# Performance work log

Measured on AMD Instinct MI355X. Metric: run time of the kernel, lower is better.

## Reference

```python
import jax, jax.numpy as jnp
import numpy as np

B, S, D, K = 4, 4096, 1024, 4
EPS = 1e-6


def rmsnorm(x, w):
    # x: [..., D]; matches torch RMSNorm: x * rsqrt(mean(x^2) + eps) * w
    n = jax.lax.rsqrt(jnp.mean(x * x, axis=-1, keepdims=True) + EPS)
    return x * n * w


def setup_inputs() -> dict:
    key = jax.random.key(0)
    ks = jax.random.split(key, 6)
    return {
        "x": jax.random.normal(ks[0], (B, S, D), jnp.float32),
        "norm_w": jnp.ones((D,), jnp.float32),
        "in_w": jax.random.normal(ks[1], (D, 2 * D), jnp.float32) / np.sqrt(D).astype(np.float32),
        "conv_w": jax.random.normal(ks[2], (D, 1, K), jnp.float32) / np.sqrt(K).astype(np.float32),
        "conv_b": jnp.zeros((D,), jnp.float32),
        "decay": jax.random.normal(ks[3], (D,), jnp.float32),
        "gate_w": jnp.ones((D,), jnp.float32),
        "out_w": jax.random.normal(ks[4], (D, D), jnp.float32) / np.sqrt(D).astype(np.float32),
        "res_scale": jnp.ones((1,), jnp.float32),
    }


def reference(x, norm_w, in_w, conv_w, conv_b, decay, gate_w, out_w, res_scale):
    residual = x
    h = rmsnorm(x, norm_w)
    xz = jnp.einsum("bsd,de->bse", h, in_w)          # [B,S,2D]
    xb, z = jnp.split(xz, 2, axis=-1)                  # each [B,S,D]

    # depthwise causal conv1d (left pad K-1, truncate to S)
    xc = jax.lax.conv_general_dilated(
        xb.transpose(0, 2, 1), conv_w,
        window_strides=(1,), padding=[(K - 1, 0)],
        feature_group_count=D,
        dimension_numbers=("NCH", "OIH", "NCH"))
    xc = (xc + conv_b[None, :, None]).transpose(0, 2, 1)  # [B,S,D]
    xc = jax.nn.silu(xc)

    # RNN cell: diagonal linear recurrence h_t = a * h_{t-1} + x_t
    a = jax.nn.sigmoid(decay)                          # [D]

    def step(hprev, xt):
        hnew = a * hprev + xt
        return hnew, hnew

    h0 = jnp.zeros((B, D), xc.dtype)
    _, hs = jax.lax.scan(step, h0, xc.transpose(1, 0, 2))  # [S,B,D]
    hs = hs.transpose(1, 0, 2)                             # [B,S,D]

    y = rmsnorm(hs, gate_w) * jax.nn.silu(z)
    y = jnp.einsum("bsd,de->bse", y, out_w)
    return residual * res_scale + y
```

## Files before the change

kernel.cpp:

```cpp
#include <hip/hip_runtime.h>
#include <cstddef>

#define BATCH 4
#define SEQ   4096
#define DIM   1024
#define KCONV 4
#define EPSV  1e-6f
#define MROWS (BATCH * SEQ)
#define CHUNK 32
#define NCHUNK (SEQ / CHUNK)

using short8v = __attribute__((ext_vector_type(8))) short;
using f32x4   = __attribute__((ext_vector_type(4))) float;

__device__ __forceinline__ unsigned short f2bf_rne(float f) {
  unsigned int u = __float_as_uint(f);
  u += 0x7FFFu + ((u >> 16) & 1u);
  return (unsigned short)(u >> 16);
}
__device__ __forceinline__ float bf2f(unsigned short h) {
  return __uint_as_float((unsigned int)h << 16);
}

__device__ __forceinline__ float wave_reduce_sum(float v) {
#pragma unroll
  for (int off = 32; off > 0; off >>= 1)
    v += __shfl_xor(v, off, 64);
  return v;
}

__global__ __launch_bounds__(256) void splitx_kernel(
    const float* __restrict__ x, const float* __restrict__ norm_w,
    unsigned short* __restrict__ Xhi, unsigned short* __restrict__ Xlo) {
  const int row = blockIdx.x * 4 + (threadIdx.x >> 6);
  const int lane = threadIdx.x & 63;
  float4 v[4];
  float ss = 0.f;
#pragma unroll
  for (int i = 0; i < 4; ++i) {
    v[i] = *reinterpret_cast<const float4*>(
        &x[(size_t)row * DIM + lane * 4 + i * 256]);
    ss += v[i].x * v[i].x + v[i].y * v[i].y + v[i].z * v[i].z + v[i].w * v[i].w;
  }
  const float rstd = rsqrtf(wave_reduce_sum(ss) * (1.0f / DIM) + EPSV);
#pragma unroll
  for (int i = 0; i < 4; ++i) {
    const int d4 = lane * 4 + i * 256;
    const float4 w = *reinterpret_cast<const float4*>(&norm_w[d4]);
    const float hv[4] = {v[i].x * rstd * w.x, v[i].y * rstd * w.y,
                         v[i].z * rstd * w.z, v[i].w * rstd * w.w};
    ushort4 hh, ll;
    hh.x = f2bf_rne(hv[0]); ll.x = f2bf_rne(hv[0] - bf2f(hh.x));
    hh.y = f2bf_rne(hv[1]); ll.y = f2bf_rne(hv[1] - bf2f(hh.y));
    hh.z = f2bf_rne(hv[2]); ll.z = f2bf_rne(hv[2] - bf2f(hh.z));
    hh.w = f2bf_rne(hv[3]); ll.w = f2bf_rne(hv[3] - bf2f(hh.w));
    *reinterpret_cast<ushort4*>(&Xhi[(size_t)row * DIM + d4]) = hh;
    *reinterpret_cast<ushort4*>(&Xlo[(size_t)row * DIM + d4]) = ll;
  }
}

__global__ __launch_bounds__(256) void splitw_kernel(
    const float* __restrict__ W, unsigned short* __restrict__ Whi,
    unsigned short* __restrict__ Wlo, int K, int N) {
  __shared__ float t[32][33];
  const int n0 = blockIdx.x * 32, k0 = blockIdx.y * 32;
  const int c = threadIdx.x & 31, r = threadIdx.x >> 5;
#pragma unroll
  for (int i = 0; i < 4; ++i)
    t[r + i * 8][c] = W[(size_t)(k0 + r + i * 8) * N + n0 + c];
  __syncthreads();
#pragma unroll
  for (int i = 0; i < 4; ++i) {
    const int n = n0 + r + i * 8, k = k0 + c;
    const float v = t[c][r + i * 8];
    const unsigned short h = f2bf_rne(v);
    Whi[(size_t)n * K + k] = h;
    Wlo[(size_t)n * K + k] = f2bf_rne(v - bf2f(h));
  }
}

template <int NT, bool RESID, bool OBF16>
__global__ __launch_bounds__(256) void gemm_kernel(
    const unsigned short* __restrict__ Ahi, const unsigned short* __restrict__ Alo,
    const unsigned short* __restrict__ Bhi, const unsigned short* __restrict__ Blo,
    float* __restrict__ Cf, unsigned short* __restrict__ Ch, int N, int lda,
    const float* __restrict__ resid, const float* __restrict__ res_scale) {
  __shared__ __align__(16) unsigned short lds[NT * 4096];

  const int tid = threadIdx.x;
  const int lane = tid & 63;
  const int wr = tid >> 7;
  const int wc = (tid >> 6) & 1;

  const int nwg = gridDim.x * gridDim.y;
  int id = blockIdx.y * gridDim.x + blockIdx.x;
  id = (id & 7) * (nwg >> 3) + (id >> 3);
  const int bx = id % gridDim.x;
  const int by = id / gridDim.x;
  const int bm = by * 128;
  const int bn = bx * 128;

  const unsigned short* pg[2 * NT];
  unsigned int lofs[2 * NT];
#pragma unroll
  for (int i = 0; i < 2 * NT; ++i) {
    const int o = tid * 16 + i * 4096;
    const int t = o >> 13;
    const int ot = o & 8191;
    const int b = ot ^ (((ot >> 7) & 7) << 4);
    const int r = b >> 6;
    const int ck = (b & 63) >> 1;
    const unsigned short* base;
    bool aside;
    if constexpr (NT == 4) {
      base = (t == 0) ? Ahi : (t == 1) ? Alo : (t == 2) ? Bhi : Blo;
      aside = (t < 2);
    } else {
      base = (t == 0) ? Ahi : Bhi;
      aside = (t < 1);
    }
    const int stride = aside ? lda : 1024;
    const int rowg = (aside ? bm : bn) + r;
    pg[i] = base + (size_t)rowg * stride + ck;
    lofs[i] = (unsigned int)(o >> 1);
  }

  unsigned int aoff[4], boff[4];
#pragma unroll
  for (int i = 0; i < 4; ++i) {
    int ba = (wr * 64 + i * 16 + (lane & 15)) * 64 + (lane >> 4) * 16;
    ba ^= ((ba >> 7) & 7) << 4;
    aoff[i] = (unsigned int)(ba >> 1);
    int bb = (wc * 64 + i * 16 + (lane & 15)) * 64 + (lane >> 4) * 16;
    bb ^= ((bb >> 7) & 7) << 4;
    boff[i] = (unsigned int)(bb >> 1) + (NT / 2) * 4096;
  }

  f32x4 acc[4][4];
#pragma unroll
  for (int mi = 0; mi < 4; ++mi)
#pragma unroll
    for (int ni = 0; ni < 4; ++ni) {
      acc[mi][ni][0] = 0.f; acc[mi][ni][1] = 0.f;
      acc[mi][ni][2] = 0.f; acc[mi][ni][3] = 0.f;
    }

  for (int k0 = 0; k0 < 1024; k0 += 32) {
#pragma unroll
    for (int i = 0; i < 2 * NT; ++i)
      __builtin_amdgcn_global_load_lds(
          (const __attribute__((address_space(1))) void*)(pg[i] + k0),
          (__attribute__((address_space(3))) void*)(&lds[lofs[i]]), 16, 0, 0);
    __syncthreads();

    short8v bh[4], bl[4];
#pragma unroll
    for (int ni = 0; ni < 4; ++ni) {
      bh[ni] = *reinterpret_cast<const short8v*>(&lds[boff[ni]]);
      if constexpr (NT == 4)
        bl[ni] = *reinterpret_cast<const short8v*>(&lds[boff[ni] + 4096]);
    }
#pragma unroll
    for (int mi = 0; mi < 4; ++mi) {
      const short8v ah = *reinterpret_cast<const short8v*>(&lds[aoff[mi]]);
#pragma unroll
      for (int ni = 0; ni < 4; ++ni)
        acc[mi][ni] = __builtin_amdgcn_mfma_f32_16x16x32_bf16(ah, bh[ni], acc[mi][ni], 0, 0, 0);
      if constexpr (NT == 4) {
        const short8v al = *reinterpret_cast<const short8v*>(&lds[aoff[mi] + 4096]);
#pragma unroll
        for (int ni = 0; ni < 4; ++ni) {
          acc[mi][ni] = __builtin_amdgcn_mfma_f32_16x16x32_bf16(ah, bl[ni], acc[mi][ni], 0, 0, 0);
          acc[mi][ni] = __builtin_amdgcn_mfma_f32_16x16x32_bf16(al, bh[ni], acc[mi][ni], 0, 0, 0);
        }
      }
    }
    __syncthreads();
  }

  const float rscale = RESID ? res_scale[0] : 0.0f;
#pragma unroll
  for (int mi = 0; mi < 4; ++mi) {
    const int row0 = bm + wr * 64 + mi * 16 + (lane >> 4) * 4;
#pragma unroll
    for (int ni = 0; ni < 4; ++ni) {
      const int col = bn + wc * 64 + ni * 16 + (lane & 15);
#pragma unroll
      for (int r = 0; r < 4; ++r) {
        const size_t idx = (size_t)(row0 + r) * N + col;
        float v = acc[mi][ni][r];
        if constexpr (RESID) v = fmaf(resid[idx], rscale, v);
        if constexpr (OBF16) Ch[idx] = f2bf_rne(v);
        else                 Cf[idx] = v;
      }
    }
  }
}

__global__ __launch_bounds__(256) void phaseA_kernel(
    const float* __restrict__ xb, const float* __restrict__ conv_w,
    const float* __restrict__ conv_b, const float* __restrict__ decay,
    float* __restrict__ hs, float* __restrict__ fbuf) {
  const int d = blockIdx.x * 256 + threadIdx.x;
  const int c = blockIdx.y;
  const int b = blockIdx.z;
  const int t0 = c * CHUNK;

  const float w0 = conv_w[d * KCONV + 0];
  const float w1 = conv_w[d * KCONV + 1];
  const float w2 = conv_w[d * KCONV + 2];
  const float w3 = conv_w[d * KCONV + 3];
  const float cb = conv_b[d];
  const float a = 1.0f / (1.0f + expf(-decay[d]));

  const size_t rowbase = ((size_t)b * SEQ + t0) * DIM + d;
  float xm1 = 0.f, xm2 = 0.f, xm3 = 0.f;
  if (t0 >= 1) xm1 = xb[rowbase - 1 * (size_t)DIM];
  if (t0 >= 2) xm2 = xb[rowbase - 2 * (size_t)DIM];
  if (t0 >= 3) xm3 = xb[rowbase - 3 * (size_t)DIM];

  float h = 0.f;
  size_t src = rowbase;
#pragma unroll 4
  for (int t = 0; t < CHUNK; ++t) {
    const float cur = xb[src];
    const float conv =
        fmaf(w0, xm3, fmaf(w1, xm2, fmaf(w2, xm1, fmaf(w3, cur, cb))));
    const float u = conv / (1.0f + expf(-conv));
    h = fmaf(a, h, u);
    hs[src] = h;
    xm3 = xm2; xm2 = xm1; xm1 = cur;
    src += DIM;
  }
  fbuf[((size_t)b * NCHUNK + c) * DIM + d] = h;
}

__global__ __launch_bounds__(256) void phaseB_kernel(
    const float* __restrict__ decay, const float* __restrict__ fbuf,
    float* __restrict__ cbuf) {
  const int d = blockIdx.x * 256 + threadIdx.x;
  const int b = blockIdx.y;
  const float a = 1.0f / (1.0f + expf(-decay[d]));
  const float aL = exp2f((float)CHUNK * __log2f(a));
  float carry = 0.f;
  for (int c = 0; c < NCHUNK; ++c) {
    const size_t idx = ((size_t)b * NCHUNK + c) * DIM + d;
    cbuf[idx] = carry;
    carry = fmaf(aL, carry, fbuf[idx]);
  }
}

__global__ __launch_bounds__(256) void phaseC_kernel(
    const unsigned short* __restrict__ z, const float* __restrict__ hs,
    const float* __restrict__ cbuf, const float* __restrict__ decay,
    const float* __restrict__ gate_w, unsigned short* __restrict__ Yhi) {
  const int row = blockIdx.x * 4 + (threadIdx.x >> 6);
  const int lane = threadIdx.x & 63;
  const int b = row >> 12;
  const int t = row & (SEQ - 1);
  const int c = t / CHUNK;
  const float e = (float)((t & (CHUNK - 1)) + 1);

  float hv[16];
  float ss = 0.f;
#pragma unroll
  for (int i = 0; i < 4; ++i) {
    const int d4 = lane * 4 + i * 256;
    const float4 dc = *reinterpret_cast<const float4*>(&decay[d4]);
    const float4 cv = *reinterpret_cast<const float4*>(
        &cbuf[((size_t)b * NCHUNK + c) * DIM + d4]);
    const float4 hl = *reinterpret_cast<const float4*>(
        &hs[(size_t)row * DIM + d4]);
    const float ad[4] = {dc.x, dc.y, dc.z, dc.w};
    const float cr[4] = {cv.x, cv.y, cv.z, cv.w};
    const float hh[4] = {hl.x, hl.y, hl.z, hl.w};
#pragma unroll
    for (int j = 0; j < 4; ++j) {
      const float a = 1.0f / (1.0f + expf(-ad[j]));
      const float ae = exp2f(e * __log2f(a));
      const float v = fmaf(ae, cr[j], hh[j]);
      hv[i * 4 + j] = v;
      ss = fmaf(v, v, ss);
    }
  }
  const float rstd = rsqrtf(wave_reduce_sum(ss) * (1.0f / DIM) + EPSV);
#pragma unroll
  for (int i = 0; i < 4; ++i) {
    const int d4 = lane * 4 + i * 256;
    const ushort4 zs = *reinterpret_cast<const ushort4*>(
        &z[(size_t)row * DIM + d4]);
    const float4 gw = *reinterpret_cast<const float4*>(&gate_w[d4]);
    const float zf[4] = {bf2f(zs.x), bf2f(zs.y), bf2f(zs.z), bf2f(zs.w)};
    const float gf[4] = {gw.x, gw.y, gw.z, gw.w};
    ushort4 yo;
    unsigned short* yp = &yo.x;
#pragma unroll
    for (int j = 0; j < 4; ++j) {
      const float sz = zf[j] / (1.0f + expf(-zf[j]));
      yp[j] = f2bf_rne(hv[i * 4 + j] * rstd * gf[j] * sz);
    }
    *reinterpret_cast<ushort4*>(&Yhi[(size_t)row * DIM + d4]) = yo;
  }
}

extern "C" void kernel_launch(void* const* d_in, const int* in_sizes, int n_in,
                              void* d_out, int out_size, void* d_ws,
                              size_t ws_size, hipStream_t stream) {
  const float* x = (const float*)d_in[0];
  const float* norm_w = (const float*)d_in[1];
  const float* in_w = (const float*)d_in[2];
  const float* conv_w = (const float*)d_in[3];
  const float* conv_b = (const float*)d_in[4];
  const float* decay = (const float*)d_in[5];
  const float* gate_w = (const float*)d_in[6];
  const float* out_w = (const float*)d_in[7];
  const float* res_scale = (const float*)d_in[8];
  float* out = (float*)d_out;

  const size_t NEEDED = 213909504;
  if (ws_size < NEEDED) return;

  char* w8 = (char*)d_ws;
  float* xb = (float*)(w8);
  unsigned short* zbf = (unsigned short*)(w8 + 67108864);
  unsigned short* yhi = (unsigned short*)(w8 + 100663296);
  unsigned short* xhi = (unsigned short*)(w8 + 134217728);
  unsigned short* xlo = (unsigned short*)(w8 + 167772160);
  float* hs = (float*)(w8 + 134217728);
  unsigned short* w1hi = (unsigned short*)(w8 + 201326592);
  unsigned short* w1lo = (unsigned short*)(w8 + 205520896);
  unsigned short* w2hi = (unsigned short*)(w8 + 209715200);
  unsigned short* w2lo = (unsigned short*)(w8 + 211812352);
  float* fbuf = (float*)d_out;
  float* cbuf = fbuf + (size_t)BATCH * NCHUNK * DIM;

  splitx_kernel<<<MROWS / 4, 256, 0, stream>>>(x, norm_w, xhi, xlo);

  splitw_kernel<<<dim3((2 * DIM) / 32, DIM / 32), 256, 0, stream>>>(
      in_w, w1hi, w1lo, DIM, 2 * DIM);
  splitw_kernel<<<dim3(DIM / 32, DIM / 32), 256, 0, stream>>>(
      out_w, w2hi, w2lo, DIM, DIM);

  gemm_kernel<4, false, false><<<dim3(8, 128), 256, 0, stream>>>(
      xhi, xlo, w1hi, w1lo, xb, nullptr, DIM, 1024, nullptr, nullptr);

  gemm_kernel<2, false, true><<<dim3(8, 128), 256, 0, stream>>>(
      xhi, nullptr, w1hi + (size_t)1024 * 1024, nullptr, nullptr, zbf,
      DIM, 1024, nullptr, nullptr);

  phaseA_kernel<<<dim3(DIM / 256, NCHUNK, BATCH), 256, 0, stream>>>(
      xb, conv_w, conv_b, decay, hs, fbuf);

  phaseB_kernel<<<dim3(DIM / 256, BATCH), 256, 0, stream>>>(decay, fbuf, cbuf);

  phaseC_kernel<<<MROWS / 4, 256, 0, stream>>>(zbf, hs, cbuf, decay, gate_w, yhi);

  gemm_kernel<2, true, false><<<dim3(8, 128), 256, 0, stream>>>(
      yhi, nullptr, w2hi, nullptr, out, nullptr, DIM, 1024, x, res_scale);
}
```

Before: 421.3 us.

## Merge weight-split launches, stagger GEMM workgroup start, batch phaseB loads

Combines the two weight bf16-split kernels into one launch using blockIdx.z to pick the matrix. It also adds a small per-workgroup s_sleep stagger at GEMM start to spread out memory requests. Finally, it unrolls the phaseB carry scan to issue 8 independent loads before the serial FMA chain. This trades launch overhead and load latency for a little idle time in the GEMM.

```diff
diff --git a/kernel.cpp b/kernel.cpp
--- a/kernel.cpp
+++ b/kernel.cpp
@@ -59,9 +59,17 @@
   }
 }
 
-__global__ __launch_bounds__(256) void splitw_kernel(
-    const float* __restrict__ W, unsigned short* __restrict__ Whi,
-    unsigned short* __restrict__ Wlo, int K, int N) {
+__global__ __launch_bounds__(256) void splitw2_kernel(
+    const float* __restrict__ W0, unsigned short* __restrict__ W0hi,
+    unsigned short* __restrict__ W0lo, const float* __restrict__ W1,
+    unsigned short* __restrict__ W1hi, unsigned short* __restrict__ W1lo) {
+  const float* W; unsigned short *Whi, *Wlo; int N;
+  if (blockIdx.z == 0) { W = W0; Whi = W0hi; Wlo = W0lo; N = 2048; }
+  else {
+    if (blockIdx.x >= 32) return;
+    W = W1; Whi = W1hi; Wlo = W1lo; N = 1024;
+  }
+  const int K = 1024;
   __shared__ float t[32][33];
   const int n0 = blockIdx.x * 32, k0 = blockIdx.y * 32;
   const int c = threadIdx.x & 31, r = threadIdx.x >> 5;
@@ -99,6 +107,13 @@
   const int by = id / gridDim.x;
   const int bm = by * 128;
   const int bn = bx * 128;
+
+  switch (id & 3) {
+    case 1: __builtin_amdgcn_s_sleep(8);  break;
+    case 2: __builtin_amdgcn_s_sleep(16); break;
+    case 3: __builtin_amdgcn_s_sleep(24); break;
+    default: break;
+  }
 
   const unsigned short* pg[2 * NT];
   unsigned int lofs[2 * NT];
@@ -242,11 +257,18 @@
   const int b = blockIdx.y;
   const float a = 1.0f / (1.0f + expf(-decay[d]));
   const float aL = exp2f((float)CHUNK * __log2f(a));
+  const float* fp = fbuf + (size_t)b * NCHUNK * DIM + d;
+  float* cp = cbuf + (size_t)b * NCHUNK * DIM + d;
   float carry = 0.f;
-  for (int c = 0; c < NCHUNK; ++c) {
-    const size_t idx = ((size_t)b * NCHUNK + c) * DIM + d;
-    cbuf[idx] = carry;
-    carry = fmaf(aL, carry, fbuf[idx]);
+  for (int c0 = 0; c0 < NCHUNK; c0 += 8) {
+    float v[8];
+#pragma unroll
+    for (int i = 0; i < 8; ++i) v[i] = fp[(size_t)(c0 + i) * DIM];
+#pragma unroll
+    for (int i = 0; i < 8; ++i) {
+      cp[(size_t)(c0 + i) * DIM] = carry;
+      carry = fmaf(aL, carry, v[i]);
+    }
   }
 }
 
@@ -336,10 +358,8 @@
 
   splitx_kernel<<<MROWS / 4, 256, 0, stream>>>(x, norm_w, xhi, xlo);
 
-  splitw_kernel<<<dim3((2 * DIM) / 32, DIM / 32), 256, 0, stream>>>(
-      in_w, w1hi, w1lo, DIM, 2 * DIM);
-  splitw_kernel<<<dim3(DIM / 32, DIM / 32), 256, 0, stream>>>(
-      out_w, w2hi, w2lo, DIM, DIM);
+  splitw2_kernel<<<dim3(64, 32, 2), 256, 0, stream>>>(
+      in_w, w1hi, w1lo, out_w, w2hi, w2lo);
 
   gemm_kernel<4, false, false><<<dim3(8, 128), 256, 0, stream>>>(
       xhi, xlo, w1hi, w1lo, xb, nullptr, DIM, 1024, nullptr, nullptr);
```

Result: faster. 411.3 us (-2.4%).
